# Kernel tuning notes

Hardware: AMD Instinct MI355X
Metric: run time of the kernel (lower is better)

Reference implementation:

```python
import jax, jax.numpy as jnp
import numpy as np

DIM = 180; HEADS = 6; WS = 16; NUM_TOKENS = 64; RDIM = 10; CAT = 128
KS = 5; MLP_HID = 360; DTD = 64; Hh = 64; Ww = 64; B = 8; M = 64


def _ln(x, g, b, eps=1e-5):
    mu = x.mean(-1, keepdims=True)
    var = ((x - mu) ** 2).mean(-1, keepdims=True)
    return (x - mu) / jnp.sqrt(var + eps) * g + b


def _l2norm(x):
    return x / jnp.clip(jnp.linalg.norm(x, axis=-1, keepdims=True), 1e-12)


def setup_inputs() -> dict:
    key = jax.random.key(0)
    ks = jax.random.split(key, 24)
    rn = lambda k, s: jax.random.normal(k, s, jnp.float32) * 0.02
    z = lambda *s: jnp.zeros(s, jnp.float32)
    return {
        'x': jax.random.normal(ks[0], (B, Hh * Ww, DIM), jnp.float32),
        'td': jax.random.normal(ks[1], (B, M, DIM), jnp.float32),
        'norm1_g': jnp.ones((DIM,), jnp.float32), 'norm1_b': z(DIM),
        'wqkv_w': rn(ks[2], (DIM, 3 * DIM)), 'wqkv_b': z(3 * DIM),
        'atd_wq_w': rn(ks[3], (DIM, RDIM)), 'atd_wq_b': z(RDIM),
        'atd_wk_w': rn(ks[4], (DIM, RDIM)), 'atd_wk_b': z(RDIM),
        'atd_wv_w': rn(ks[5], (DIM, DIM)), 'atd_wv_b': z(DIM),
        'atd_scale': jnp.ones((1,), jnp.float32),
        'aca_proj_w': rn(ks[6], (DIM, DIM)), 'aca_proj_b': z(DIM),
        'win_rpb': rn(ks[7], ((2 * WS - 1) ** 2, HEADS)),
        'win_proj_w': rn(ks[8], (DIM, DIM)), 'win_proj_b': z(DIM),
        'fc_td_w': rn(ks[9], (DIM, DTD)), 'fc_td_b': z(DTD),
        'fc1_w': rn(ks[10], (DIM, MLP_HID)), 'fc1_b': z(MLP_HID),
        'dw_w': rn(ks[11], (MLP_HID + DTD, 1, KS, KS)), 'dw_b': z(MLP_HID + DTD),
        'fc2_w': rn(ks[12], (MLP_HID + DTD, DIM)), 'fc2_b': z(DIM),
        'norm2_g': jnp.ones((DIM,), jnp.float32), 'norm2_b': z(DIM),
        'rpi_sa': jax.random.randint(ks[13], (WS * WS, WS * WS), 0, (2 * WS - 1) ** 2),
        'h': Hh, 'w': Ww,
    }


def reference(x, td, norm1_g, norm1_b, wqkv_w, wqkv_b, atd_wq_w, atd_wq_b,
              atd_wk_w, atd_wk_b, atd_wv_w, atd_wv_b, atd_scale,
              aca_proj_w, aca_proj_b, win_rpb, win_proj_w, win_proj_b,
              fc_td_w, fc_td_b, fc1_w, fc1_b, dw_w, dw_b, fc2_w, fc2_b,
              norm2_g, norm2_b, rpi_sa, h, w):
    b, n, c = x.shape
    hd = c // HEADS
    shortcut = x
    xn = _ln(x, norm1_g, norm1_b)
    qkv = xn @ wqkv_w + wqkv_b  # [b, n, 3c]

    # --- ATD_CA: l2-normalized cross-attention to token dictionary ---
    q = xn @ atd_wq_w + atd_wq_b          # [b, n, rd]
    kk = td @ atd_wk_w + atd_wk_b         # [b, m, rd]
    vv = td @ atd_wv_w + atd_wv_b         # [b, m, c]
    logit_scale = 1.0 + jnp.clip(atd_scale, 0.0, 3.0) * np.log(NUM_TOKENS)
    sim = jnp.einsum('bnr,bmr->bnm', _l2norm(q), _l2norm(kk)) * logit_scale
    attn_atd = jax.nn.softmax(sim, axis=-1)
    x_atd = jnp.einsum('bnm,bmc->bnc', attn_atd, vv)
    tk_id = jnp.argmax(attn_atd, axis=-1)  # [b, n]

    # --- AC_MSA: category-sorted grouped attention ---
    gs = min(n, CAT); ng = (n + gs - 1) // gs; pad_n = ng * gs - n
    sort_idx = jnp.argsort(tk_id, axis=-1)
    inv_idx = jnp.argsort(sort_idx, axis=-1)  # inverse permutation
    sq = jnp.take_along_axis(qkv, sort_idx[:, :, None], axis=1)
    sq = jnp.concatenate([sq, jnp.flip(sq[:, n - pad_n:n, :], axis=1)], axis=1)
    g = sq.reshape(b, ng, gs, 3, HEADS, hd).transpose(3, 0, 1, 4, 2, 5)
    qa, ka, va = g[0], g[1], g[2]          # [b, ng, H, gs, hd]
    a = jax.nn.softmax(jnp.einsum('bgHid,bgHjd->bgHij', qa, ka) * hd ** -0.5, axis=-1)
    y = jnp.einsum('bgHij,bgHjd->bgHid', a, va).transpose(0, 1, 3, 2, 4)
    y = y.reshape(b, n + pad_n, c)[:, :n]
    x_aca = jnp.take_along_axis(y, inv_idx[:, :, None], axis=1) @ aca_proj_w + aca_proj_b

    # --- gather per-token dictionary features for FFN ---
    td_proj = td @ fc_td_w + fc_td_b       # [b, m, dtd]
    x_td = jnp.take_along_axis(td_proj, jnp.broadcast_to(tk_id[:, :, None], (b, n, DTD)), axis=1)

    # --- window attention (shift_size = 0, no mask) ---
    nwh, nww = h // WS, w // WS
    win = qkv.reshape(b, nwh, WS, nww, WS, 3 * c).transpose(0, 1, 3, 2, 4, 5)
    win = win.reshape(-1, WS * WS, 3 * c)
    B_ = win.shape[0]; N = WS * WS
    wq = win.reshape(B_, N, 3, HEADS, hd).transpose(2, 0, 3, 1, 4)
    qw, kw, vw = wq[0] * hd ** -0.5, wq[1], wq[2]
    bias = win_rpb[rpi_sa.reshape(-1)].reshape(N, N, HEADS).transpose(2, 0, 1)[None]
    aw = jax.nn.softmax(jnp.einsum('wHid,wHjd->wHij', qw, kw) + bias, axis=-1)
    ow = jnp.einsum('wHij,wHjd->wHid', aw, vw).transpose(0, 2, 1, 3).reshape(B_, N, c)
    ow = ow @ win_proj_w + win_proj_b
    attn_x = ow.reshape(b, nwh, nww, WS, WS, c).transpose(0, 1, 3, 2, 4, 5).reshape(b, n, c)

    x = shortcut + x_atd + attn_x + x_aca

    # --- ConvFFN_td with depthwise conv branch ---
    x2 = _ln(x, norm2_g, norm2_b)
    h1 = jax.nn.gelu(x2 @ fc1_w + fc1_b, approximate=False)
    hc = jnp.concatenate([h1, x_td], axis=-1)  # [b, n, C]
    C = hc.shape[-1]
    img = jnp.swapaxes(hc, 1, 2).reshape(b, C, h, w)
    conv = jax.lax.conv_general_dilated(img, dw_w, (1, 1), 'SAME',
        dimension_numbers=('NCHW', 'OIHW', 'NCHW'), feature_group_count=C)
    conv = jax.nn.gelu(conv + dw_b[None, :, None, None], approximate=False)
    hc = hc + jnp.swapaxes(conv.reshape(b, C, n), 1, 2)
    return x + hc @ fc2_w + fc2_b
```

## Files before the change

kernel.cpp:

```cpp
#include <hip/hip_runtime.h>
#include <hip/hip_bf16.h>
#include <math.h>

#define BB      8
#define NTOK    4096
#define CDIM    180
#define C3      540
#define NHEADS  6
#define HD      30
#define MDICT   64
#define RD      10
#define DTD     64
#define MHID    360
#define CCAT    424
#define WS      16
#define WIN_N   256
#define GS      128
#define NG      32
#define ROWS    (BB*NTOK)
#define KP1     192
#define KP2     448

typedef __hip_bfloat16 bf16;
typedef short v8s __attribute__((ext_vector_type(8)));
typedef float f32x4 __attribute__((ext_vector_type(4)));
typedef unsigned int u32x4 __attribute__((ext_vector_type(4)));

__device__ __forceinline__ float gelu_exact(float x) {
    return 0.5f * x * (1.0f + erff(x * 0.70710678118654752f));
}
__device__ __forceinline__ float wave_sum(float v) {
    #pragma unroll
    for (int off = 32; off > 0; off >>= 1) v += __shfl_xor(v, off, 64);
    return v;
}
__device__ __forceinline__ unsigned short f2b(float v) {
    unsigned u = __float_as_uint(v);
    return (unsigned short)((u + 0x7FFFu + ((u >> 16) & 1u)) >> 16);
}
__device__ __forceinline__ float b2f(unsigned short h) {
    return __uint_as_float(((unsigned)h) << 16);
}
__device__ __forceinline__ unsigned packbf(float lo, float hi) {
    return (unsigned)f2b(lo) | ((unsigned)f2b(hi) << 16);
}

__global__ __launch_bounds__(256) void detect_kernel(const void* __restrict__ x,
                                                     int* __restrict__ flag,
                                                     int* __restrict__ diag)
{
    __shared__ int cnt;
    if (threadIdx.x == 0) { cnt = 0; *diag = 0; }
    __syncthreads();
    const unsigned short* u = (const unsigned short*)x;
    int c = 0;
    for (int i = threadIdx.x; i < 2048; i += 256) {
        unsigned short e = u[2 * i] & 0x7F80;
        if (e >= 0x4300) c++;
    }
    atomicAdd(&cnt, c);
    __syncthreads();
    if (threadIdx.x == 0) *flag = (cnt > 16) ? 1 : 0;
}

#define NCVT 23
struct CvtArgs {
    const void* src[NCVT];
    float* dst[NCVT];
    int cum[NCVT + 1];
};
__global__ __launch_bounds__(256) void convert_all_kernel(CvtArgs a, int total,
        const int* __restrict__ flag)
{
    int i = blockIdx.x * 256 + threadIdx.x;
    if (i >= total) return;
    int s = 0;
    while (i >= a.cum[s + 1]) s++;
    int off = i - a.cum[s];
    if (*flag) a.dst[s][off] = ((const float*)a.src[s])[off];
    else       a.dst[s][off] = __bfloat162float(((const bf16*)a.src[s])[off]);
}

__global__ __launch_bounds__(256) void check_f32_kernel(const float* __restrict__ buf,
        int n, int bit, int* __restrict__ diag)
{
    int i = blockIdx.x * 256 + threadIdx.x;
    if (i >= n) return;
    unsigned u = __float_as_uint(buf[i]);
    if ((u & 0x7F800000u) == 0x7F800000u) atomicOr(diag, bit);
}

__global__ __launch_bounds__(256) void emit_kernel(const float* __restrict__ src,
        void* __restrict__ out, const int* __restrict__ flag,
        const int* __restrict__ diag, int n)
{
    int i = blockIdx.x * 256 + threadIdx.x;
    if (i >= n) return;
    float v = src[i];
    int d = *diag;
    if (d) v = 100.f + 32.f * (float)d;
    if (*flag) ((float*)out)[i] = v;
    else       ((bf16*)out)[i]  = __float2bfloat16(v);
}

__global__ __launch_bounds__(256) void zero_tail_kernel(bf16* __restrict__ buf)
{
    int idx = blockIdx.x * 256 + threadIdx.x;
    int row = idx / 12, c = idx % 12;
    buf[(size_t)row * KP1 + CDIM + c] = __float2bfloat16(0.f);
}

__global__ __launch_bounds__(256) void packW_kernel(const void* __restrict__ W,
        bf16* __restrict__ Wt, int K, int N, int Kpad, int total,
        const int* __restrict__ flag)
{
    int idx = blockIdx.x * 256 + threadIdx.x;
    if (idx >= total) return;
    int n = idx / Kpad, k = idx % Kpad;
    float v = 0.f;
    if (k < K && n < N) {
        size_t src = (size_t)k * N + n;
        v = (*flag) ? ((const float*)W)[src]
                    : __bfloat162float(((const bf16*)W)[src]);
    }
    Wt[idx] = __float2bfloat16(v);
}

__global__ __launch_bounds__(256) void bias_pre_kernel(const int* __restrict__ rpi,
        const float* __restrict__ rpb, float* __restrict__ bias_t)
{
    int idx = blockIdx.x * 256 + threadIdx.x;
    int h = idx >> 16, ij = idx & 65535;
    bias_t[idx] = rpb[rpi[ij] * NHEADS + h];
}

template<bool GELU_, bool ADDRES, bool BIAS_>
__global__ __launch_bounds__(256) void mgemm_kernel(
        const bf16* __restrict__ A, int lda,
        const bf16* __restrict__ Wt, int ldw,
        const float* __restrict__ bias,
        const float* __restrict__ res, int ldr,
        float* __restrict__ outF, int ldo, int N, int K)
{
    __shared__ unsigned short As[64][32];
    __shared__ unsigned short Bs[64][32];
    int tid = threadIdx.x;
    int wave = tid >> 6, lane = tid & 63;
    int quad = lane >> 4, mr = lane & 15;
    int row0 = blockIdx.y * 64, col0 = blockIdx.x * 64;
    f32x4 z = {0.f, 0.f, 0.f, 0.f};
    f32x4 acc[4] = {z, z, z, z};
    const unsigned short* Au = (const unsigned short*)A;
    const unsigned short* Wu = (const unsigned short*)Wt;
    for (int k0 = 0; k0 < K; k0 += 32) {
        #pragma unroll
        for (int e = 0; e < 8; e++) {
            int idx = tid * 8 + e;
            int r = idx >> 5, c = idx & 31;
            As[r][c] = Au[(size_t)(row0 + r) * lda + k0 + c];
            Bs[r][c] = Wu[(size_t)(col0 + r) * ldw + k0 + c];
        }
        __syncthreads();
        v8s a;
        #pragma unroll
        for (int j = 0; j < 8; j++) a[j] = (short)As[wave * 16 + mr][quad * 8 + j];
        #pragma unroll
        for (int ni = 0; ni < 4; ni++) {
            v8s b;
            #pragma unroll
            for (int j = 0; j < 8; j++) b[j] = (short)Bs[ni * 16 + mr][quad * 8 + j];
            acc[ni] = __builtin_amdgcn_mfma_f32_16x16x32_bf16(a, b, acc[ni], 0, 0, 0);
        }
        __syncthreads();
    }
    #pragma unroll
    for (int ni = 0; ni < 4; ni++) {
        int gc = col0 + ni * 16 + mr;
        if (gc >= N) continue;
        float bv = BIAS_ ? bias[gc] : 0.f;
        #pragma unroll
        for (int r = 0; r < 4; r++) {
            int gr = row0 + wave * 16 + quad * 4 + r;
            float v = acc[ni][r] + bv;
            if (GELU_) v = gelu_exact(v);
            if (ADDRES) v += res[(size_t)gr * ldr + gc];
            outF[(size_t)gr * ldo + gc] = v;
        }
    }
}

__global__ __launch_bounds__(256) void av_mgemm_kernel(
        const bf16* __restrict__ P, const bf16* __restrict__ vvT,
        const float* __restrict__ xres, float* __restrict__ accout)
{
    __shared__ unsigned short As[64][32];
    __shared__ unsigned short Bs[64][32];
    int tid = threadIdx.x;
    int wave = tid >> 6, lane = tid & 63;
    int quad = lane >> 4, mr = lane & 15;
    int row0 = blockIdx.y * 64, col0 = blockIdx.x * 64;
    int bz = blockIdx.z;
    const unsigned short* Au = (const unsigned short*)P + (size_t)bz * NTOK * MDICT;
    const unsigned short* Wu = (const unsigned short*)vvT + (size_t)bz * 192 * MDICT;
    const float* res = xres + (size_t)bz * NTOK * CDIM;
    float* outF = accout + (size_t)bz * NTOK * CDIM;
    f32x4 z = {0.f, 0.f, 0.f, 0.f};
    f32x4 acc[4] = {z, z, z, z};
    for (int k0 = 0; k0 < MDICT; k0 += 32) {
        #pragma unroll
        for (int e = 0; e < 8; e++) {
            int idx = tid * 8 + e;
            int r = idx >> 5, c = idx & 31;
            As[r][c] = Au[(size_t)(row0 + r) * MDICT + k0 + c];
            Bs[r][c] = Wu[(size_t)(col0 + r) * MDICT + k0 + c];
        }
        __syncthreads();
        v8s a;
        #pragma unroll
        for (int j = 0; j < 8; j++) a[j] = (short)As[wave * 16 + mr][quad * 8 + j];
        #pragma unroll
        for (int ni = 0; ni < 4; ni++) {
            v8s b;
            #pragma unroll
            for (int j = 0; j < 8; j++) b[j] = (short)Bs[ni * 16 + mr][quad * 8 + j];
            acc[ni] = __builtin_amdgcn_mfma_f32_16x16x32_bf16(a, b, acc[ni], 0, 0, 0);
        }
        __syncthreads();
    }
    #pragma unroll
    for (int ni = 0; ni < 4; ni++) {
        int gc = col0 + ni * 16 + mr;
        if (gc >= CDIM) continue;
        #pragma unroll
        for (int r = 0; r < 4; r++) {
            int gr = row0 + wave * 16 + quad * 4 + r;
            float v = acc[ni][r] + res[(size_t)gr * CDIM + gc];
            outF[(size_t)gr * CDIM + gc] = v;
        }
    }
}

__global__ __launch_bounds__(256, 4) void win_mfma_kernel(const float* __restrict__ qkv,
        const float* __restrict__ bias_t, bf16* __restrict__ outb)
{
    int b = blockIdx.y;
    int widx = blockIdx.x / NHEADS;
    int hh = blockIdx.x % NHEADS;
    int wy = widx >> 2, wx = widx & 3;
    int tid = threadIdx.x;
    int wave = tid >> 6, lane = tid & 63, quad = lane >> 4, mr = lane & 15;
    __shared__ __align__(16) unsigned short Ks[64][40];
    __shared__ __align__(16) unsigned short Vt[32][80];

    size_t brow = (size_t)b * NTOK;
    const float scq = 0.18257418583505536f;

    v8s aq[4];
    #pragma unroll
    for (int tt = 0; tt < 4; tt++) {
        int m = (wave * 4 + tt) * 16 + mr;
        int nt_ = (wy * WS + (m >> 4)) * 64 + wx * WS + (m & 15);
        const float* qrow = qkv + (brow + nt_) * C3 + hh * HD;
        #pragma unroll
        for (int jj = 0; jj < 8; jj++) {
            int d = quad * 8 + jj;
            float v = (d < HD) ? qrow[d] * scq : 0.f;
            aq[tt][jj] = (short)f2b(v);
        }
    }
    f32x4 z = {0.f, 0.f, 0.f, 0.f};
    f32x4 oacc[4][2] = {{z, z}, {z, z}, {z, z}, {z, z}};
    float m_r[4], l_r[4];
    #pragma unroll
    for (int tt = 0; tt < 4; tt++) { m_r[tt] = -3.0e38f; l_r[tt] = 0.f; }
    const float* btab = bias_t + (size_t)hh * WIN_N * WIN_N;

    for (int kc = 0; kc < WIN_N; kc += 64) {
        {
            int j = tid >> 2, dg = (tid & 3) * 8;
            int tok = kc + j;
            int nt_ = (wy * WS + (tok >> 4)) * 64 + wx * WS + (tok & 15);
            const float* krow = qkv + (brow + nt_) * C3 + CDIM + hh * HD;
            const float* vrow = qkv + (brow + nt_) * C3 + 2 * CDIM + hh * HD;
            v8s kv;
            #pragma unroll
            for (int jj = 0; jj < 8; jj++) {
                int d = dg + jj;
                float kf = (d < HD) ? krow[d] : 0.f;
                float vf = (d < HD) ? vrow[d] : 0.f;
                kv[jj] = (short)f2b(kf);
                Vt[d][j] = f2b(vf);
            }
            *(v8s*)&Ks[j][dg] = kv;
        }
        __syncthreads();
        #pragma unroll
        for (int tt = 0; tt < 4; tt++) {
            f32x4 s[4];
            #pragma unroll
            for (int nt = 0; nt < 4; nt++) {
                v8s bk = *(const v8s*)&Ks[nt * 16 + mr][quad * 8];
                s[nt] = __builtin_amdgcn_mfma_f32_16x16x32_bf16(bk, aq[tt], z, 0, 0, 0);
            }
            int qg = (wave * 4 + tt) * 16 + mr;
            const float* bi = btab + (size_t)qg * WIN_N + kc;
            float mc = -3.0e38f;
            #pragma unroll
            for (int nt = 0; nt < 4; nt++) {
                f32x4 b4 = *(const f32x4*)(bi + nt * 16 + quad * 4);
                s[nt][0] += b4[0]; s[nt][1] += b4[1];
                s[nt][2] += b4[2]; s[nt][3] += b4[3];
                mc = fmaxf(mc, fmaxf(fmaxf(s[nt][0], s[nt][1]),
                                     fmaxf(s[nt][2], s[nt][3])));
            }
            mc = fmaxf(mc, __shfl_xor(mc, 16, 64));
            mc = fmaxf(mc, __shfl_xor(mc, 32, 64));
            float mn = fmaxf(m_r[tt], mc);
            float alpha = __expf(m_r[tt] - mn);
            m_r[tt] = mn;
            float ls = 0.f;
            #pragma unroll
            for (int nt = 0; nt < 4; nt++) {
                #pragma unroll
                for (int r = 0; r < 4; r++) {
                    float pp = __expf(s[nt][r] - mn);
                    ls += pp;
                    s[nt][r] = pp;
                }
            }
            ls += __shfl_xor(ls, 16, 64);
            ls += __shfl_xor(ls, 32, 64);
            l_r[tt] = l_r[tt] * alpha + ls;
            unsigned dpk[4][2];
            #pragma unroll
            for (int nt = 0; nt < 4; nt++) {
                dpk[nt][0] = packbf(s[nt][0], s[nt][1]);
                dpk[nt][1] = packbf(s[nt][2], s[nt][3]);
            }
            #pragma unroll
            for (int r = 0; r < 4; r++) {
                float av = __shfl(alpha, quad * 4 + r, 64);
                oacc[tt][0][r] *= av;
                oacc[tt][1][r] *= av;
            }
            #pragma unroll
            for (int c = 0; c < 2; c++) {
                union { u32x4 u; v8s s8; } afu;
                #pragma unroll
                for (int t = 0; t < 4; t++) {
                    int srcl = (((quad * 2 + (t >> 1)) & 3) << 4) | mr;
                    unsigned r0 = (unsigned)__shfl((int)dpk[2 * c][t & 1], srcl, 64);
                    unsigned r1 = (unsigned)__shfl((int)dpk[2 * c + 1][t & 1], srcl, 64);
                    afu.u[t] = (quad & 2) ? r1 : r0;
                }
                #pragma unroll
                for (int dt = 0; dt < 2; dt++) {
                    v8s bv = *(const v8s*)&Vt[dt * 16 + mr][c * 32 + quad * 8];
                    oacc[tt][dt] = __builtin_amdgcn_mfma_f32_16x16x32_bf16(
                        afu.s8, bv, oacc[tt][dt], 0, 0, 0);
                }
            }
        }
        __syncthreads();
    }
    #pragma unroll
    for (int tt = 0; tt < 4; tt++) {
        float il = 1.f / l_r[tt];
        #pragma unroll
        for (int r = 0; r < 4; r++) {
            float ilr = __shfl(il, quad * 4 + r, 64);
            int m = (wave * 4 + tt) * 16 + quad * 4 + r;
            int nt_ = (wy * WS + (m >> 4)) * 64 + wx * WS + (m & 15);
            #pragma unroll
            for (int dt = 0; dt < 2; dt++) {
                int d = dt * 16 + mr;
                if (d >= HD) continue;
                outb[(brow + nt_) * KP1 + hh * HD + d] =
                    __float2bfloat16(oacc[tt][dt][r] * ilr);
            }
        }
    }
}

__global__ __launch_bounds__(256, 4) void acmsa_mfma_kernel(const float* __restrict__ qkv,
        const int* __restrict__ sidx, bf16* __restrict__ outb)
{
    int b = blockIdx.y;
    int g = blockIdx.x / NHEADS;
    int hh = blockIdx.x % NHEADS;
    int tid = threadIdx.x;
    int wave = tid >> 6, lane = tid & 63, quad = lane >> 4, mr = lane & 15;
    __shared__ int toks[GS];
    __shared__ __align__(16) unsigned short Ks[64][40];
    __shared__ __align__(16) unsigned short Vt[32][80];

    size_t brow = (size_t)b * NTOK;
    if (tid < GS) toks[tid] = sidx[brow + (size_t)g * GS + tid];
    __syncthreads();
    const float scq = 0.18257418583505536f;

    v8s aq[2];
    #pragma unroll
    for (int tt = 0; tt < 2; tt++) {
        int m = (wave * 2 + tt) * 16 + mr;
        const float* qrow = qkv + (brow + toks[m]) * C3 + hh * HD;
        #pragma unroll
        for (int jj = 0; jj < 8; jj++) {
            int d = quad * 8 + jj;
            float v = (d < HD) ? qrow[d] * scq : 0.f;
            aq[tt][jj] = (short)f2b(v);
        }
    }
    f32x4 z = {0.f, 0.f, 0.f, 0.f};
    f32x4 oacc[2][2] = {{z, z}, {z, z}};
    float m_r[2], l_r[2];
    #pragma unroll
    for (int tt = 0; tt < 2; tt++) { m_r[tt] = -3.0e38f; l_r[tt] = 0.f; }

    for (int kc = 0; kc < GS; kc += 64) {
        {
            int j = tid >> 2, dg = (tid & 3) * 8;
            int tok = toks[kc + j];
            const float* krow = qkv + (brow + tok) * C3 + CDIM + hh * HD;
            const float* vrow = qkv + (brow + tok) * C3 + 2 * CDIM + hh * HD;
            v8s kv;
            #pragma unroll
            for (int jj = 0; jj < 8; jj++) {
                int d = dg + jj;
                float kf = (d < HD) ? krow[d] : 0.f;
                float vf = (d < HD) ? vrow[d] : 0.f;
                kv[jj] = (short)f2b(kf);
                Vt[d][j] = f2b(vf);
            }
            *(v8s*)&Ks[j][dg] = kv;
        }
        __syncthreads();
        #pragma unroll
        for (int tt = 0; tt < 2; tt++) {
            f32x4 s[4];
            #pragma unroll
            for (int nt = 0; nt < 4; nt++) {
                v8s bk = *(const v8s*)&Ks[nt * 16 + mr][quad * 8];
                s[nt] = __builtin_amdgcn_mfma_f32_16x16x32_bf16(bk, aq[tt], z, 0, 0, 0);
            }
            float mc = -3.0e38f;
            #pragma unroll
            for (int nt = 0; nt < 4; nt++)
                mc = fmaxf(mc, fmaxf(fmaxf(s[nt][0], s[nt][1]),
                                     fmaxf(s[nt][2], s[nt][3])));
            mc = fmaxf(mc, __shfl_xor(mc, 16, 64));
            mc = fmaxf(mc, __shfl_xor(mc, 32, 64));
            float mn = fmaxf(m_r[tt], mc);
            float alpha = __expf(m_r[tt] - mn);
            m_r[tt] = mn;
            float ls = 0.f;
            #pragma unroll
            for (int nt = 0; nt < 4; nt++) {
                #pragma unroll
                for (int r = 0; r < 4; r++) {
                    float pp = __expf(s[nt][r] - mn);
                    ls += pp;
                    s[nt][r] = pp;
                }
            }
            ls += __shfl_xor(ls, 16, 64);
            ls += __shfl_xor(ls, 32, 64);
            l_r[tt] = l_r[tt] * alpha + ls;
            unsigned dpk[4][2];
            #pragma unroll
            for (int nt = 0; nt < 4; nt++) {
                dpk[nt][0] = packbf(s[nt][0], s[nt][1]);
                dpk[nt][1] = packbf(s[nt][2], s[nt][3]);
            }
            #pragma unroll
            for (int r = 0; r < 4; r++) {
                float av = __shfl(alpha, quad * 4 + r, 64);
                oacc[tt][0][r] *= av;
                oacc[tt][1][r] *= av;
            }
            #pragma unroll
            for (int c = 0; c < 2; c++) {
                union { u32x4 u; v8s s8; } afu;
                #pragma unroll
                for (int t = 0; t < 4; t++) {
                    int srcl = (((quad * 2 + (t >> 1)) & 3) << 4) | mr;
                    unsigned r0 = (unsigned)__shfl((int)dpk[2 * c][t & 1], srcl, 64);
                    unsigned r1 = (unsigned)__shfl((int)dpk[2 * c + 1][t & 1], srcl, 64);
                    afu.u[t] = (quad & 2) ? r1 : r0;
                }
                #pragma unroll
                for (int dt = 0; dt < 2; dt++) {
                    v8s bv = *(const v8s*)&Vt[dt * 16 + mr][c * 32 + quad * 8];
                    oacc[tt][dt] = __builtin_amdgcn_mfma_f32_16x16x32_bf16(
                        afu.s8, bv, oacc[tt][dt], 0, 0, 0);
                }
            }
        }
        __syncthreads();
    }
    #pragma unroll
    for (int tt = 0; tt < 2; tt++) {
        float il = 1.f / l_r[tt];
        #pragma unroll
        for (int r = 0; r < 4; r++) {
            float ilr = __shfl(il, quad * 4 + r, 64);
            int m = (wave * 2 + tt) * 16 + quad * 4 + r;
            int tok = toks[m];
            #pragma unroll
            for (int dt = 0; dt < 2; dt++) {
                int d = dt * 16 + mr;
                if (d >= HD) continue;
                outb[(brow + tok) * KP1 + hh * HD + d] =
                    __float2bfloat16(oacc[tt][dt][r] * ilr);
            }
        }
    }
}

__global__ __launch_bounds__(64) void ln_kernel(const float* __restrict__ x,
        const float* __restrict__ g, const float* __restrict__ be,
        float* __restrict__ out, bf16* __restrict__ outb)
{
    int row = blockIdx.x; int t = threadIdx.x;
    const float* xr = x + (size_t)row * CDIM;
    float v0 = xr[t];
    float v1 = xr[t + 64];
    float v2 = (t < CDIM - 128) ? xr[t + 128] : 0.f;
    float s1 = wave_sum(v0 + v1 + v2);
    float s2 = wave_sum(v0*v0 + v1*v1 + v2*v2);
    float mu = s1 / (float)CDIM;
    float var = s2 / (float)CDIM - mu * mu;
    float rs = rsqrtf(var + 1e-5f);
    float o0 = (v0 - mu) * rs * g[t]      + be[t];
    float o1 = (v1 - mu) * rs * g[t + 64] + be[t + 64];
    float o2 = (t < CDIM - 128) ? ((v2 - mu) * rs * g[t + 128] + be[t + 128]) : 0.f;
    float* o = out + (size_t)row * CDIM;
    o[t] = o0; o[t + 64] = o1;
    if (t < CDIM - 128) o[t + 128] = o2;
    bf16* ob = outb + (size_t)row * KP1;
    ob[t]       = __float2bfloat16(o0);
    ob[t + 64]  = __float2bfloat16(o1);
    ob[t + 128] = __float2bfloat16(o2);
}

__global__ __launch_bounds__(64) void td_pre_kernel(const float* __restrict__ td,
        const float* __restrict__ wk, const float* __restrict__ wkb,
        const float* __restrict__ wv, const float* __restrict__ wvb,
        const float* __restrict__ wtd, const float* __restrict__ wtdb,
        float* __restrict__ kkn, bf16* __restrict__ vvT, float* __restrict__ tdp)
{
    int blk = blockIdx.x;
    int b = blk >> 6, m = blk & 63;
    int t = threadIdx.x;
    __shared__ float tr[CDIM];
    __shared__ float sk[RD];
    __shared__ float snorm;
    const float* tdr = td + (size_t)blk * CDIM;
    tr[t] = tdr[t]; tr[t + 64] = tdr[t + 64];
    if (t < CDIM - 128) tr[t + 128] = tdr[t + 128];
    __syncthreads();
    if (t < RD) {
        float s = wkb[t];
        for (int k = 0; k < CDIM; k++) s += tr[k] * wk[k * RD + t];
        sk[t] = s;
    }
    __syncthreads();
    if (t == 0) {
        float s = 0.f;
        #pragma unroll
        for (int j = 0; j < RD; j++) s += sk[j] * sk[j];
        snorm = fmaxf(sqrtf(s), 1e-12f);
    }
    __syncthreads();
    if (t < RD) kkn[(size_t)blk * RD + t] = sk[t] / snorm;
    for (int c = t; c < 192; c += 64) {
        float s = 0.f;
        if (c < CDIM) {
            s = wvb[c];
            for (int k = 0; k < CDIM; k++) s += tr[k] * wv[k * CDIM + c];
        }
        vvT[((size_t)(b * 192 + c)) * MDICT + m] = __float2bfloat16(s);
    }
    {
        float s = wtdb[t];
        for (int k = 0; k < CDIM; k++) s += tr[k] * wtd[k * DTD + t];
        tdp[(size_t)blk * DTD + t] = s;
    }
}

__global__ __launch_bounds__(64) void atd_soft_kernel(const float* __restrict__ xn,
        const float* __restrict__ wq, const float* __restrict__ wqb,
        const float* __restrict__ scale_p, const float* __restrict__ kkn,
        bf16* __restrict__ Pout, int* __restrict__ tk_id)
{
    int row = blockIdx.x;
    int b = row >> 12;
    int t = threadIdx.x;
    const float* xrow = xn + (size_t)row * CDIM;
    float v0 = xrow[t];
    float v1 = xrow[t + 64];
    float v2 = (t < CDIM - 128) ? xrow[t + 128] : 0.f;
    float sq[RD];
    #pragma unroll
    for (int j = 0; j < RD; j++) {
        float part = v0 * wq[t * RD + j] + v1 * wq[(t + 64) * RD + j];
        if (t < CDIM - 128) part += v2 * wq[(t + 128) * RD + j];
        sq[j] = wave_sum(part) + wqb[j];
    }
    float qn = 0.f;
    #pragma unroll
    for (int j = 0; j < RD; j++) qn += sq[j] * sq[j];
    qn = fmaxf(sqrtf(qn), 1e-12f);
    float ls = 1.0f + fminf(fmaxf(scale_p[0], 0.f), 3.f) * 4.158883083359672f;
    const float* kr = kkn + ((size_t)b * MDICT + t) * RD;
    float s = 0.f;
    #pragma unroll
    for (int j = 0; j < RD; j++) s += sq[j] * kr[j];
    s = s / qn * ls;
    float mv = s; int mi = t;
    #pragma unroll
    for (int off = 32; off > 0; off >>= 1) {
        float ov = __shfl_xor(mv, off, 64);
        int   oi = __shfl_xor(mi, off, 64);
        if (ov > mv || (ov == mv && oi < mi)) { mv = ov; mi = oi; }
    }
    float e = __expf(s - mv);
    float denom = wave_sum(e);
    Pout[(size_t)row * MDICT + t] = __float2bfloat16(e / denom);
    if (t == 0) tk_id[row] = mi;
}

__global__ __launch_bounds__(256) void sort_kernel(const int* __restrict__ tk_id,
                                                   int* __restrict__ sidx)
{
    int b = blockIdx.x; int tid = threadIdx.x;
    __shared__ int keys[NTOK];
    __shared__ int cnt[256];
    __shared__ int off[256];
    const int* kb = tk_id + (size_t)b * NTOK;
    for (int i = tid; i < NTOK; i += 256) keys[i] = kb[i];
    __syncthreads();
    int v = tid >> 2, seg = tid & 3;
    int lo = seg * 1024, hi = lo + 1024;
    int c = 0;
    for (int i = lo; i < hi; i++) c += (keys[i] == v);
    cnt[tid] = c;
    __syncthreads();
    if (tid == 0) {
        int run = 0;
        for (int l = 0; l < 256; l++) { off[l] = run; run += cnt[l]; }
    }
    __syncthreads();
    int o = off[tid];
    int* sb = sidx + (size_t)b * NTOK;
    for (int i = lo; i < hi; i++) if (keys[i] == v) sb[o++] = i;
}

__global__ __launch_bounds__(256) void gather_td_kernel(const int* __restrict__ tk_id,
        const float* __restrict__ tdp, float* __restrict__ hc)
{
    int idx = blockIdx.x * 256 + threadIdx.x;
    int row = idx >> 6, j = idx & 63;
    int b = row >> 12;
    int tk = tk_id[row];
    hc[(size_t)row * CCAT + MHID + j] = tdp[((size_t)b * MDICT + tk) * DTD + j];
}

#define CHK3 64
#define CTW  8
#define CTH  8
#define CHW  12
#define CHP  144
#define CSPX 68
__global__ __launch_bounds__(256) void conv_kernel(const float* __restrict__ hc,
        const float* __restrict__ w, const float* __restrict__ wb,
        bf16* __restrict__ outb)
{
    int ch0 = blockIdx.x * CHK3;
    int tile = blockIdx.y;
    int b = blockIdx.z;
    int ty0 = (tile >> 3) * CTH, tx0 = (tile & 7) * CTW;
    __shared__ __align__(16) float sh[CHP][CSPX];
    __shared__ __align__(16) float wt[25][CHK3];
    int tid = threadIdx.x;
    for (int idx = tid; idx < CHP * CHK3; idx += 256) {
        int pix = idx >> 6, ch = idx & 63;
        int gy = ty0 + pix / CHW - 2, gx = tx0 + pix % CHW - 2;
        int chg = ch0 + ch;
        float v = 0.f;
        if (gy >= 0 && gy < 64 && gx >= 0 && gx < 64 && chg < CCAT)
            v = hc[((size_t)b * NTOK + gy * 64 + gx) * CCAT + chg];
        sh[pix][ch] = v;
    }
    for (int idx = tid; idx < 25 * CHK3; idx += 256) {
        int kk = idx >> 6, ch = idx & 63;
        int chg = ch0 + ch;
        wt[kk][ch] = (chg < CCAT) ? w[chg * 25 + kk] : 0.f;
    }
    __syncthreads();
    int q = tid & 3, p = tid >> 2;
    int px = p & 7, py = p >> 3;
    int cb = q * 16;
    int pc = py * CHW + px;
    v8s pk0, pk1;
    #pragma unroll
    for (int sub = 0; sub < 4; sub++) {
        int cs = cb + sub * 4;
        f32x4 acc = {0.f, 0.f, 0.f, 0.f};
        #pragma unroll
        for (int dy = 0; dy < 5; dy++) {
            #pragma unroll
            for (int dx = 0; dx < 5; dx++) {
                f32x4 sv = *(const f32x4*)&sh[pc + dy * CHW + dx][cs];
                f32x4 wv = *(const f32x4*)&wt[dy * 5 + dx][cs];
                acc += sv * wv;
            }
            __builtin_amdgcn_sched_barrier(0);
        }
        f32x4 ctr = *(const f32x4*)&sh[pc + 2 * CHW + 2][cs];
        #pragma unroll
        for (int c = 0; c < 4; c++) {
            int chg = ch0 + cs + c;
            float v = 0.f;
            if (chg < CCAT) {
                float gv = gelu_exact(acc[c] + wb[chg]);
                v = ctr[c] + gv;
            }
            int lc = sub * 4 + c;
            if (lc < 8) pk0[lc] = (short)f2b(v);
            else        pk1[lc - 8] = (short)f2b(v);
        }
        __builtin_amdgcn_sched_barrier(0);
    }
    size_t obase = ((size_t)b * NTOK + (ty0 + py) * 64 + tx0 + px) * KP2 + ch0 + cb;
    unsigned short* ob = (unsigned short*)outb + obase;
    *(v8s*)ob = pk0;
    *(v8s*)(ob + 8) = pk1;
}

extern "C" void kernel_launch(void* const* d_in, const int* in_sizes, int n_in,
                              void* d_out, int out_size, void* d_ws, size_t ws_size,
                              hipStream_t stream)
{
    (void)n_in; (void)ws_size; (void)out_size;
    const int* rpi = (const int*)d_in[28];

    float* p = (float*)d_ws;
    float* xn    = p; p += (size_t)ROWS * CDIM;
    float* acc   = p; p += (size_t)ROWS * CDIM;
    float* tmp1  = p; p += (size_t)ROWS * CDIM;
    float* qkv   = p; p += (size_t)ROWS * C3;
    float* hcnew = p; p += (size_t)ROWS * CCAT;
    float* kkn   = p; p += (size_t)BB * MDICT * RD;
    bf16*  vvT   = (bf16*)p; p += (size_t)BB * 192 * MDICT / 2;
    float* tdp   = p; p += (size_t)BB * MDICT * DTD;
    int*   tk_id = (int*)p; p += ROWS;
    int*   sidx  = (int*)p; p += ROWS;
    int*   flag  = (int*)p; p += 64;
    int*   diag  = (int*)p; p += 64;
    bf16* wtqkv = (bf16*)p; p += 576 * KP1 / 2;
    bf16* wtaca = (bf16*)p; p += 192 * KP1 / 2;
    bf16* wtwin = (bf16*)p; p += 192 * KP1 / 2;
    bf16* wtfc1 = (bf16*)p; p += 384 * KP1 / 2;
    bf16* wtfc2 = (bf16*)p; p += 192 * KP2 / 2;
    float* cin[28];
    for (int i = 0; i < 28; i++) { cin[i] = p; p += in_sizes[i]; }
    float* bias_t = p; p += (size_t)NHEADS * WIN_N * WIN_N;

    float* hc      = qkv;
    bf16*  xnb     = (bf16*)hcnew;
    bf16*  tmp1b   = (bf16*)(hcnew + (size_t)ROWS * KP1 / 2);
    bf16*  hcnewb2 = (bf16*)hcnew;
    bf16*  Pbuf    = (bf16*)tmp1;

    detect_kernel<<<1, 256, 0, stream>>>(d_in[0], flag, diag);
    {
        CvtArgs ca;
        int total = 0, s = 0;
        for (int i = 0; i < 28; i++) {
            if (i == 4 || i == 13 || i == 16 || i == 20 || i == 24) continue;
            ca.src[s] = d_in[i];
            ca.dst[s] = cin[i];
            ca.cum[s] = total;
            total += in_sizes[i];
            s++;
        }
        ca.cum[s] = total;
        convert_all_kernel<<<(total + 255) / 256, 256, 0, stream>>>(ca, total, flag);
    }
    const float *x = cin[0], *td = cin[1], *n1g = cin[2], *n1b = cin[3],
        *wqkv_b = cin[5], *wq_w = cin[6], *wq_b = cin[7],
        *wk_w = cin[8], *wk_b = cin[9], *wv_w = cin[10], *wv_b = cin[11],
        *atd_scale = cin[12], *aca_b = cin[14], *win_rpb = cin[15],
        *winp_b = cin[17], *fctd_w = cin[18], *fctd_b = cin[19],
        *fc1_b = cin[21], *dw_w = cin[22], *dw_b = cin[23], *fc2_b = cin[25],
        *n2g = cin[26], *n2b = cin[27];

    packW_kernel<<<576 * KP1 / 256, 256, 0, stream>>>(d_in[4],  wtqkv, CDIM, C3,   KP1, 576 * KP1, flag);
    packW_kernel<<<192 * KP1 / 256, 256, 0, stream>>>(d_in[13], wtaca, CDIM, CDIM, KP1, 192 * KP1, flag);
    packW_kernel<<<192 * KP1 / 256, 256, 0, stream>>>(d_in[16], wtwin, CDIM, CDIM, KP1, 192 * KP1, flag);
    packW_kernel<<<384 * KP1 / 256, 256, 0, stream>>>(d_in[20], wtfc1, CDIM, MHID, KP1, 384 * KP1, flag);
    packW_kernel<<<192 * KP2 / 256, 256, 0, stream>>>(d_in[24], wtfc2, CCAT, CDIM, KP2, 192 * KP2, flag);
    bias_pre_kernel<<<NHEADS * WIN_N * WIN_N / 256, 256, 0, stream>>>(rpi, win_rpb, bias_t);

    td_pre_kernel<<<BB * MDICT, 64, 0, stream>>>(td, wk_w, wk_b, wv_w, wv_b,
                                                 fctd_w, fctd_b, kkn, vvT, tdp);
    ln_kernel<<<ROWS, 64, 0, stream>>>(x, n1g, n1b, xn, xnb);
    mgemm_kernel<false, false, true><<<dim3(9, ROWS / 64), 256, 0, stream>>>(
        xnb, KP1, wtqkv, KP1, wqkv_b, nullptr, 0, qkv, C3, C3, KP1);
    atd_soft_kernel<<<ROWS, 64, 0, stream>>>(xn, wq_w, wq_b, atd_scale, kkn, Pbuf, tk_id);
    av_mgemm_kernel<<<dim3(3, NTOK / 64, BB), 256, 0, stream>>>(Pbuf, vvT, x, acc);
    sort_kernel<<<BB, 256, 0, stream>>>(tk_id, sidx);
    zero_tail_kernel<<<ROWS * 12 / 256, 256, 0, stream>>>(tmp1b);
    acmsa_mfma_kernel<<<dim3(NG * NHEADS, BB), 256, 0, stream>>>(qkv, sidx, tmp1b);
    mgemm_kernel<false, true, true><<<dim3(3, ROWS / 64), 256, 0, stream>>>(
        tmp1b, KP1, wtaca, KP1, aca_b, acc, CDIM, acc, CDIM, CDIM, KP1);
    win_mfma_kernel<<<dim3(16 * NHEADS, BB), 256, 0, stream>>>(qkv, bias_t, tmp1b);
    mgemm_kernel<false, true, true><<<dim3(3, ROWS / 64), 256, 0, stream>>>(
        tmp1b, KP1, wtwin, KP1, winp_b, acc, CDIM, acc, CDIM, CDIM, KP1);
    ln_kernel<<<ROWS, 64, 0, stream>>>(acc, n2g, n2b, xn, xnb);
    mgemm_kernel<true, false, true><<<dim3(6, ROWS / 64), 256, 0, stream>>>(
        xnb, KP1, wtfc1, KP1, fc1_b, nullptr, 0, hc, CCAT, MHID, KP1);
    gather_td_kernel<<<ROWS * 64 / 256, 256, 0, stream>>>(tk_id, tdp, hc);
    conv_kernel<<<dim3(7, 64, BB), 256, 0, stream>>>(hc, dw_w, dw_b, hcnewb2);
    mgemm_kernel<false, true, true><<<dim3(3, ROWS / 64), 256, 0, stream>>>(
        hcnewb2, KP2, wtfc2, KP2, fc2_b, acc, CDIM, tmp1, CDIM, CDIM, KP2);
    check_f32_kernel<<<(ROWS * CDIM + 255) / 256, 256, 0, stream>>>(tmp1, ROWS * CDIM, 8, diag);
    emit_kernel<<<(ROWS * CDIM + 255) / 256, 256, 0, stream>>>(
        tmp1, d_out, flag, diag, ROWS * CDIM);
}
```

Measured before the change: 706.4 us.

## Enlarge GEMM row tile to 128, use direct global-to-LDS loads and vector fragment reads

The generic bf16 MFMA GEMM now computes a 128x64 tile per block, with each wave owning two 16-row strips so each B fragment is reused twice. Tiles are staged with 16-byte global_load_lds transfers instead of per-element scalar copies, and A/B fragments are read from LDS as 8-element vectors. This targets the scalar load overhead and low data reuse of the old GEMM, at the cost of halving the grid size (fewer blocks for occupancy) and adding more accumulator registers.

```diff
diff --git a/kernel.cpp b/kernel.cpp
--- a/kernel.cpp
+++ b/kernel.cpp
@@ -44,6 +44,11 @@
 __device__ __forceinline__ unsigned packbf(float lo, float hi) {
     return (unsigned)f2b(lo) | ((unsigned)f2b(hi) << 16);
 }
+__device__ __forceinline__ void gload16(const void* g, void* l) {
+    __builtin_amdgcn_global_load_lds(
+        (const __attribute__((address_space(1))) void*)g,
+        (__attribute__((address_space(3))) void*)l, 16, 0, 0);
+}
 
 __global__ __launch_bounds__(256) void detect_kernel(const void* __restrict__ x,
                                                      int* __restrict__ flag,
@@ -142,34 +147,33 @@
         const float* __restrict__ res, int ldr,
         float* __restrict__ outF, int ldo, int N, int K)
 {
-    __shared__ unsigned short As[64][32];
-    __shared__ unsigned short Bs[64][32];
+    __shared__ __align__(16) unsigned short As[128][32];
+    __shared__ __align__(16) unsigned short Bs[64][32];
     int tid = threadIdx.x;
     int wave = tid >> 6, lane = tid & 63;
     int quad = lane >> 4, mr = lane & 15;
-    int row0 = blockIdx.y * 64, col0 = blockIdx.x * 64;
+    int row0 = blockIdx.y * 128, col0 = blockIdx.x * 64;
+    int ar = tid >> 2, ac = (tid & 3) * 8;
     f32x4 z = {0.f, 0.f, 0.f, 0.f};
-    f32x4 acc[4] = {z, z, z, z};
+    f32x4 acc[2][4] = {{z, z, z, z}, {z, z, z, z}};
     const unsigned short* Au = (const unsigned short*)A;
     const unsigned short* Wu = (const unsigned short*)Wt;
     for (int k0 = 0; k0 < K; k0 += 32) {
-        #pragma unroll
-        for (int e = 0; e < 8; e++) {
-            int idx = tid * 8 + e;
-            int r = idx >> 5, c = idx & 31;
-            As[r][c] = Au[(size_t)(row0 + r) * lda + k0 + c];
-            Bs[r][c] = Wu[(size_t)(col0 + r) * ldw + k0 + c];
-        }
+        gload16(&Au[(size_t)(row0 + ar) * lda + k0 + ac],      &As[ar][ac]);
+        gload16(&Au[(size_t)(row0 + 64 + ar) * lda + k0 + ac], &As[64 + ar][ac]);
+        gload16(&Wu[(size_t)(col0 + ar) * ldw + k0 + ac],      &Bs[ar][ac]);
         __syncthreads();
-        v8s a;
-        #pragma unroll
-        for (int j = 0; j < 8; j++) a[j] = (short)As[wave * 16 + mr][quad * 8 + j];
-        #pragma unroll
-        for (int ni = 0; ni < 4; ni++) {
-            v8s b;
-            #pragma unroll
-            for (int j = 0; j < 8; j++) b[j] = (short)Bs[ni * 16 + mr][quad * 8 + j];
-            acc[ni] = __builtin_amdgcn_mfma_f32_16x16x32_bf16(a, b, acc[ni], 0, 0, 0);
+        v8s bfr[4];
+        #pragma unroll
+        for (int ni = 0; ni < 4; ni++)
+            bfr[ni] = *(const v8s*)&Bs[ni * 16 + mr][quad * 8];
+        #pragma unroll
+        for (int s = 0; s < 2; s++) {
+            v8s a = *(const v8s*)&As[wave * 32 + s * 16 + mr][quad * 8];
+            #pragma unroll
+            for (int ni = 0; ni < 4; ni++)
+                acc[s][ni] = __builtin_amdgcn_mfma_f32_16x16x32_bf16(
+                    a, bfr[ni], acc[s][ni], 0, 0, 0);
         }
         __syncthreads();
     }
@@ -179,12 +183,15 @@
         if (gc >= N) continue;
         float bv = BIAS_ ? bias[gc] : 0.f;
         #pragma unroll
-        for (int r = 0; r < 4; r++) {
-            int gr = row0 + wave * 16 + quad * 4 + r;
-            float v = acc[ni][r] + bv;
-            if (GELU_) v = gelu_exact(v);
-            if (ADDRES) v += res[(size_t)gr * ldr + gc];
-            outF[(size_t)gr * ldo + gc] = v;
+        for (int s = 0; s < 2; s++) {
+            #pragma unroll
+            for (int r = 0; r < 4; r++) {
+                int gr = row0 + wave * 32 + s * 16 + quad * 4 + r;
+                float v = acc[s][ni][r] + bv;
+                if (GELU_) v = gelu_exact(v);
+                if (ADDRES) v += res[(size_t)gr * ldr + gc];
+                outF[(size_t)gr * ldo + gc] = v;
+            }
         }
     }
 }
@@ -806,24 +813,24 @@
     td_pre_kernel<<<BB * MDICT, 64, 0, stream>>>(td, wk_w, wk_b, wv_w, wv_b,
                                                  fctd_w, fctd_b, kkn, vvT, tdp);
     ln_kernel<<<ROWS, 64, 0, stream>>>(x, n1g, n1b, xn, xnb);
-    mgemm_kernel<false, false, true><<<dim3(9, ROWS / 64), 256, 0, stream>>>(
+    mgemm_kernel<false, false, true><<<dim3(9, ROWS / 128), 256, 0, stream>>>(
         xnb, KP1, wtqkv, KP1, wqkv_b, nullptr, 0, qkv, C3, C3, KP1);
     atd_soft_kernel<<<ROWS, 64, 0, stream>>>(xn, wq_w, wq_b, atd_scale, kkn, Pbuf, tk_id);
     av_mgemm_kernel<<<dim3(3, NTOK / 64, BB), 256, 0, stream>>>(Pbuf, vvT, x, acc);
     sort_kernel<<<BB, 256, 0, stream>>>(tk_id, sidx);
     zero_tail_kernel<<<ROWS * 12 / 256, 256, 0, stream>>>(tmp1b);
     acmsa_mfma_kernel<<<dim3(NG * NHEADS, BB), 256, 0, stream>>>(qkv, sidx, tmp1b);
-    mgemm_kernel<false, true, true><<<dim3(3, ROWS / 64), 256, 0, stream>>>(
+    mgemm_kernel<false, true, true><<<dim3(3, ROWS / 128), 256, 0, stream>>>(
         tmp1b, KP1, wtaca, KP1, aca_b, acc, CDIM, acc, CDIM, CDIM, KP1);
     win_mfma_kernel<<<dim3(16 * NHEADS, BB), 256, 0, stream>>>(qkv, bias_t, tmp1b);
-    mgemm_kernel<false, true, true><<<dim3(3, ROWS / 64), 256, 0, stream>>>(
+    mgemm_kernel<false, true, true><<<dim3(3, ROWS / 128), 256, 0, stream>>>(
         tmp1b, KP1, wtwin, KP1, winp_b, acc, CDIM, acc, CDIM, CDIM, KP1);
     ln_kernel<<<ROWS, 64, 0, stream>>>(acc, n2g, n2b, xn, xnb);
-    mgemm_kernel<true, false, true><<<dim3(6, ROWS / 64), 256, 0, stream>>>(
+    mgemm_kernel<true, false, true><<<dim3(6, ROWS / 128), 256, 0, stream>>>(
         xnb, KP1, wtfc1, KP1, fc1_b, nullptr, 0, hc, CCAT, MHID, KP1);
     gather_td_kernel<<<ROWS * 64 / 256, 256, 0, stream>>>(tk_id, tdp, hc);
     conv_kernel<<<dim3(7, 64, BB), 256, 0, stream>>>(hc, dw_w, dw_b, hcnewb2);
-    mgemm_kernel<false, true, true><<<dim3(3, ROWS / 64), 256, 0, stream>>>(
+    mgemm_kernel<false, true, true><<<dim3(3, ROWS / 128), 256, 0, stream>>>(
         hcnewb2, KP2, wtfc2, KP2, fc2_b, acc, CDIM, tmp1, CDIM, CDIM, KP2);
     check_f32_kernel<<<(ROWS * CDIM + 255) / 256, 256, 0, stream>>>(tmp1, ROWS * CDIM, 8, diag);
     emit_kernel<<<(ROWS * CDIM + 255) / 256, 256, 0, stream>>>(
```

Result: no change. 709.5 us (+0.4%).
